# Optimization experiments

Hardware: AMD Instinct MI355X
Metric: run time of the kernel (lower is better)

The kernel has to match this reference:

```python
import jax, jax.numpy as jnp
import numpy as np

N = 10000
C = 16
AVG_DEG = 32
TAU = 1.0


def _label_propagate(adj, labels, train_mask, gumbel, iter_step, k_hop):
    # Faithful port of ContextLabel.LabelPropagate + get_label_distribution.
    m = train_mask[:, None]  # [N,1] bool
    Y = jnp.where(m, labels, jnp.zeros_like(labels))  # Y_pred init: zeros w/ train rows set
    for _ in range(iter_step):
        Y = adj @ Y                      # [N,N]@[N,C] propagation (memory-bound, C small)
        Y = jnp.where(m, labels, Y)      # masked overwrite of train rows
    if k_hop == 0:
        return Y
    # F.gumbel_softmax(Y, hard=True), tau=1: straight-through one-hot
    logits = (Y + gumbel) / TAU
    soft = jax.nn.softmax(logits, axis=-1)
    hard = jax.nn.one_hot(jnp.argmax(logits, axis=-1), C, dtype=soft.dtype)
    Y = hard + soft - jax.lax.stop_gradient(soft)
    Y = jnp.where(m, labels, Y)
    # k-hop adjacency power (loop over static k_hop-1)
    a = adj
    for _ in range(k_hop - 1):
        a = a @ adj
    # get_label_distribution: torch builds a dense [N,N,C] tensor with labels[j] at every
    # nonzero (i,j) of a, then sums over dim=1. That is exactly (a != 0).float() @ labels,
    # with no gradient through the nonzero pattern — computed without the N*N*C intermediate.
    mask = jax.lax.stop_gradient((a != 0).astype(Y.dtype))
    dist = mask @ Y  # [N,C] sum of neighbor label vectors
    dist = dist / jnp.sum(dist, axis=1, keepdims=True)
    return dist


def _make_adj(key):
    k1, k2 = jax.random.split(key)
    pattern = jax.random.uniform(k1, (N, N)) < (AVG_DEG / N)  # ~32 neighbors/row
    vals = jax.random.uniform(k2, (N, N))
    a = jnp.where(pattern, vals, 0.0).astype(jnp.float32)
    a = a.at[jnp.arange(N), jnp.arange(N)].set(1.0)  # self-loops -> no empty rows
    return a / jnp.sum(a, axis=1, keepdims=True)     # row-normalized


def setup_inputs() -> dict:
    key = jax.random.key(0)
    ka, kn, kl, km, kg1, kg2 = jax.random.split(key, 6)
    adj = _make_adj(ka)             # the (perturbed) adjacency passed to forward
    adj_norm = _make_adj(kn)        # the fixed adjacency used in __init__
    labels_int = jax.random.randint(kl, (N,), 0, C)
    labels_onehot = jax.nn.one_hot(labels_int, C, dtype=jnp.float32)
    train_mask = jax.random.uniform(km, (N,)) < 0.1
    # gumbel noise: -log(-log(U)), U clipped away from {0,1}
    def gum(k):
        u = jax.random.uniform(k, (N, C), minval=1e-6, maxval=1.0 - 1e-6)
        return -jnp.log(-jnp.log(u))
    gumbel_init = gum(kg1)
    gumbel = gum(kg2)
    # pseudo_labels = detached LabelPropagate(adj_norm, labels_onehot) from __init__
    pseudo_labels = _label_propagate(adj_norm, labels_onehot, train_mask, gumbel_init,
                                     iter_step=10, k_hop=1)
    return {"adj": adj, "labels_onehot": labels_onehot, "pseudo_labels": pseudo_labels,
            "gumbel": gumbel, "train_mask": train_mask, "iter_step": 10, "k_hop": 1}


def reference(adj, labels_onehot, pseudo_labels, gumbel, train_mask, iter_step, k_hop):
    out = _label_propagate(adj, labels_onehot, train_mask, gumbel, iter_step, k_hop)
    return jnp.mean((out - pseudo_labels) ** 2)  # F.mse_loss(..., reduction='mean')
```

## Files before the change

### kernel.cpp

```cpp
#include <hip/hip_runtime.h>

#define NN 10000
#define CC 16
#define CAP 96

__device__ __forceinline__ bool mask_at(const void* p, int i, int mode) {
    if (mode == 0) return ((const int*)p)[i] != 0;
    if (mode == 1) return ((const unsigned char*)p)[i] != 0;
    return ((const float*)p)[i] != 0.0f;
}

__global__ void detect_mask_mode(const unsigned int* __restrict__ m, int* flag) {
    __shared__ int s_int_bad, s_flt_bad;
    if (threadIdx.x == 0) { s_int_bad = 0; s_flt_bad = 0; }
    __syncthreads();
    for (int i = threadIdx.x; i < NN / 4; i += blockDim.x) {
        unsigned w = m[i];
        if (w > 1u) s_int_bad = 1;
        if (w != 0u && w != 0x3F800000u) s_flt_bad = 1;
    }
    __syncthreads();
    if (threadIdx.x == 0) {
        int mode;
        if (!s_int_bad)      mode = 0;
        else if (!s_flt_bad) mode = 2;
        else                 mode = 1;
        *flag = mode;
    }
}

__global__ __launch_bounds__(256) void build_csr(const float* __restrict__ adj,
                                                 int* __restrict__ cols,
                                                 float* __restrict__ vals,
                                                 int* __restrict__ cnt) {
    __shared__ int lcnt;
    const int row = blockIdx.x;
    if (threadIdx.x == 0) lcnt = 0;
    __syncthreads();
    const float4* rp = (const float4*)(adj + (size_t)row * NN);
    const int base = row * CAP;
    for (int i = threadIdx.x; i < NN / 4; i += 256) {
        float4 v = rp[i];
        int j = i * 4;
        if (v.x != 0.f) { int p = atomicAdd(&lcnt, 1); if (p < CAP) { cols[base+p] = j;   vals[base+p] = v.x; } }
        if (v.y != 0.f) { int p = atomicAdd(&lcnt, 1); if (p < CAP) { cols[base+p] = j+1; vals[base+p] = v.y; } }
        if (v.z != 0.f) { int p = atomicAdd(&lcnt, 1); if (p < CAP) { cols[base+p] = j+2; vals[base+p] = v.z; } }
        if (v.w != 0.f) { int p = atomicAdd(&lcnt, 1); if (p < CAP) { cols[base+p] = j+3; vals[base+p] = v.w; } }
    }
    __syncthreads();
    if (threadIdx.x == 0) cnt[row] = (lcnt < CAP) ? lcnt : CAP;
}

__global__ void init_y(const float* __restrict__ labels, const void* __restrict__ tmask,
                       const int* __restrict__ flag, float* __restrict__ Y) {
    int t = blockIdx.x * 256 + threadIdx.x;
    int row = t >> 4;
    bool m = mask_at(tmask, row, *flag);
    Y[t] = m ? labels[t] : 0.0f;
}

__global__ __launch_bounds__(256) void spmv_step(const int* __restrict__ cols,
                                                 const float* __restrict__ vals,
                                                 const int* __restrict__ cnt,
                                                 const float* __restrict__ Yin,
                                                 const float* __restrict__ labels,
                                                 const void* __restrict__ tmask,
                                                 const int* __restrict__ flag,
                                                 float* __restrict__ Yout) {
    int t = blockIdx.x * 256 + threadIdx.x;
    int row = t >> 4, c = t & 15;
    int n = cnt[row];
    const int*   cp = cols + row * CAP;
    const float* vp = vals + row * CAP;
    float acc = 0.0f;
    for (int k = 0; k < n; k++) acc = fmaf(vp[k], Yin[cp[k] * CC + c], acc);
    bool m = mask_at(tmask, row, *flag);
    Yout[t] = m ? labels[t] : acc;
}

__global__ void harden(const float* __restrict__ Yin, const float* __restrict__ gumbel,
                       const float* __restrict__ labels, const void* __restrict__ tmask,
                       const int* __restrict__ flag, float* __restrict__ Yout) {
    int row = blockIdx.x * blockDim.x + threadIdx.x;
    if (row >= NN) return;
    float l[CC];
    float mx = -1e30f;
    int am = 0;
    for (int c = 0; c < CC; c++) {
        l[c] = Yin[row * CC + c] + gumbel[row * CC + c];
        if (l[c] > mx) { mx = l[c]; am = c; }
    }
    float e[CC], s = 0.0f;
    for (int c = 0; c < CC; c++) { e[c] = expf(l[c] - mx); s += e[c]; }
    bool m = mask_at(tmask, row, *flag);
    for (int c = 0; c < CC; c++) {
        float soft = e[c] / s;
        float hard = (c == am) ? 1.0f : 0.0f;
        float y = (hard + soft) - soft;
        Yout[row * CC + c] = m ? labels[row * CC + c] : y;
    }
}

__global__ __launch_bounds__(256) void mask_spmv_loss(const int* __restrict__ cols,
                                                      const int* __restrict__ cnt,
                                                      const float* __restrict__ Y2,
                                                      const float* __restrict__ pseudo,
                                                      float* __restrict__ out) {
    int t = blockIdx.x * 256 + threadIdx.x;
    int row = t >> 4;
    int n = cnt[row];
    const int* cp = cols + row * CAP;
    float acc = 0.0f;
    for (int k = 0; k < n; k++) acc += Y2[cp[k] * CC + (t & 15)];
    float rs = acc;
    for (int off = 8; off >= 1; off >>= 1) rs += __shfl_xor(rs, off, 16);
    float v = acc / rs;
    float d = v - pseudo[t];
    float contrib = d * d * (1.0f / (NN * CC));
    for (int off = 32; off >= 1; off >>= 1) contrib += __shfl_down(contrib, off, 64);
    if ((threadIdx.x & 63) == 0) atomicAdd(out, contrib);
}

extern "C" void kernel_launch(void* const* d_in, const int* in_sizes, int n_in,
                              void* d_out, int out_size, void* d_ws, size_t ws_size,
                              hipStream_t stream) {
    const float* adj    = (const float*)d_in[0];
    const float* labels = (const float*)d_in[1];
    const float* pseudo = (const float*)d_in[2];
    const float* gumbel = (const float*)d_in[3];
    const void*  tmask  = d_in[4];

    char* ws = (char*)d_ws;
    int*   flag = (int*)(ws + 0);
    int*   cnt  = (int*)(ws + 64);
    int*   cols = (int*)(ws + 40064);
    float* vals = (float*)(ws + 3880064);
    float* Ya   = (float*)(ws + 7720064);
    float* Yb   = (float*)(ws + 8360064);

    float* outp = (float*)d_out;
    hipMemsetAsync(outp, 0, sizeof(float), stream);

    detect_mask_mode<<<1, 256, 0, stream>>>((const unsigned int*)tmask, flag);
    build_csr<<<NN, 256, 0, stream>>>(adj, cols, vals, cnt);
    init_y<<<(NN * CC) / 256, 256, 0, stream>>>(labels, tmask, flag, Ya);

    float* cur = Ya;
    float* nxt = Yb;
    for (int it = 0; it < 10; ++it) {
        spmv_step<<<(NN * CC) / 256, 256, 0, stream>>>(cols, vals, cnt, cur, labels, tmask, flag, nxt);
        float* tmp = cur; cur = nxt; nxt = tmp;
    }
    harden<<<(NN + 255) / 256, 256, 0, stream>>>(cur, gumbel, labels, tmask, flag, nxt);
    mask_spmv_loss<<<(NN * CC) / 256, 256, 0, stream>>>(cols, cnt, nxt, pseudo, outp);
}
```

Baseline: 773.1 us.

## Pack CSR entries, fuse mask detection and init, replace atomic loss reduction

Column indices and values are stored together as int2 pairs so each neighbor needs one load. Mask-mode detection moves into an extra block of build_csr, and Y initialisation is folded into a first SpMV step that reads labels directly, which removes two kernel launches and one iteration. The loss switches from a global atomicAdd plus memset to per-block partial sums and a final reduction kernel, and the inner loops get unroll pragmas. Total time is dominated by the dense 400MB adjacency scan in build_csr, which is unchanged, so these launch and gather savings are small by comparison.

```diff
diff --git a/kernel.cpp b/kernel.cpp
--- a/kernel.cpp
+++ b/kernel.cpp
@@ -3,6 +3,7 @@
 #define NN 10000
 #define CC 16
 #define CAP 96
+#define NBLK 625
 
 __device__ __forceinline__ bool mask_at(const void* p, int i, int mode) {
     if (mode == 0) return ((const int*)p)[i] != 0;
@@ -10,57 +11,71 @@
     return ((const float*)p)[i] != 0.0f;
 }
 
-__global__ void detect_mask_mode(const unsigned int* __restrict__ m, int* flag) {
-    __shared__ int s_int_bad, s_flt_bad;
-    if (threadIdx.x == 0) { s_int_bad = 0; s_flt_bad = 0; }
-    __syncthreads();
-    for (int i = threadIdx.x; i < NN / 4; i += blockDim.x) {
-        unsigned w = m[i];
-        if (w > 1u) s_int_bad = 1;
-        if (w != 0u && w != 0x3F800000u) s_flt_bad = 1;
+__global__ __launch_bounds__(256) void build_csr(const float* __restrict__ adj,
+                                                 int2* __restrict__ pack,
+                                                 int* __restrict__ cnt,
+                                                 const unsigned int* __restrict__ mask_words,
+                                                 int* __restrict__ flag) {
+    if (blockIdx.x == NN) {
+        __shared__ int s_int_bad, s_flt_bad;
+        if (threadIdx.x == 0) { s_int_bad = 0; s_flt_bad = 0; }
+        __syncthreads();
+        for (int i = threadIdx.x; i < NN / 4; i += 256) {
+            unsigned w = mask_words[i];
+            if (w > 1u) s_int_bad = 1;
+            if (w != 0u && w != 0x3F800000u) s_flt_bad = 1;
+        }
+        __syncthreads();
+        if (threadIdx.x == 0) {
+            int mode;
+            if (!s_int_bad)      mode = 0;
+            else if (!s_flt_bad) mode = 2;
+            else                 mode = 1;
+            *flag = mode;
+        }
+        return;
     }
-    __syncthreads();
-    if (threadIdx.x == 0) {
-        int mode;
-        if (!s_int_bad)      mode = 0;
-        else if (!s_flt_bad) mode = 2;
-        else                 mode = 1;
-        *flag = mode;
-    }
-}
-
-__global__ __launch_bounds__(256) void build_csr(const float* __restrict__ adj,
-                                                 int* __restrict__ cols,
-                                                 float* __restrict__ vals,
-                                                 int* __restrict__ cnt) {
     __shared__ int lcnt;
     const int row = blockIdx.x;
     if (threadIdx.x == 0) lcnt = 0;
     __syncthreads();
     const float4* rp = (const float4*)(adj + (size_t)row * NN);
-    const int base = row * CAP;
+    int2* pb = pack + row * CAP;
     for (int i = threadIdx.x; i < NN / 4; i += 256) {
         float4 v = rp[i];
         int j = i * 4;
-        if (v.x != 0.f) { int p = atomicAdd(&lcnt, 1); if (p < CAP) { cols[base+p] = j;   vals[base+p] = v.x; } }
-        if (v.y != 0.f) { int p = atomicAdd(&lcnt, 1); if (p < CAP) { cols[base+p] = j+1; vals[base+p] = v.y; } }
-        if (v.z != 0.f) { int p = atomicAdd(&lcnt, 1); if (p < CAP) { cols[base+p] = j+2; vals[base+p] = v.z; } }
-        if (v.w != 0.f) { int p = atomicAdd(&lcnt, 1); if (p < CAP) { cols[base+p] = j+3; vals[base+p] = v.w; } }
+        if (v.x != 0.f) { int p = atomicAdd(&lcnt, 1); if (p < CAP) pb[p] = make_int2(j,     __float_as_int(v.x)); }
+        if (v.y != 0.f) { int p = atomicAdd(&lcnt, 1); if (p < CAP) pb[p] = make_int2(j + 1, __float_as_int(v.y)); }
+        if (v.z != 0.f) { int p = atomicAdd(&lcnt, 1); if (p < CAP) pb[p] = make_int2(j + 2, __float_as_int(v.z)); }
+        if (v.w != 0.f) { int p = atomicAdd(&lcnt, 1); if (p < CAP) pb[p] = make_int2(j + 3, __float_as_int(v.w)); }
     }
     __syncthreads();
     if (threadIdx.x == 0) cnt[row] = (lcnt < CAP) ? lcnt : CAP;
 }
 
-__global__ void init_y(const float* __restrict__ labels, const void* __restrict__ tmask,
-                       const int* __restrict__ flag, float* __restrict__ Y) {
+__global__ __launch_bounds__(256) void spmv_first(const int2* __restrict__ pack,
+                                                  const int* __restrict__ cnt,
+                                                  const float* __restrict__ labels,
+                                                  const void* __restrict__ tmask,
+                                                  const int* __restrict__ flag,
+                                                  float* __restrict__ Yout) {
     int t = blockIdx.x * 256 + threadIdx.x;
-    int row = t >> 4;
-    bool m = mask_at(tmask, row, *flag);
-    Y[t] = m ? labels[t] : 0.0f;
+    int row = t >> 4, c = t & 15;
+    int n = cnt[row];
+    int mode = *flag;
+    const int2* pp = pack + row * CAP;
+    float acc = 0.0f;
+    #pragma unroll 4
+    for (int k = 0; k < n; k++) {
+        int2 e = pp[k];
+        float yv = mask_at(tmask, e.x, mode) ? labels[e.x * CC + c] : 0.0f;
+        acc = fmaf(__int_as_float(e.y), yv, acc);
+    }
+    bool m = mask_at(tmask, row, mode);
+    Yout[t] = m ? labels[t] : acc;
 }
 
-__global__ __launch_bounds__(256) void spmv_step(const int* __restrict__ cols,
-                                                 const float* __restrict__ vals,
+__global__ __launch_bounds__(256) void spmv_step(const int2* __restrict__ pack,
                                                  const int* __restrict__ cnt,
                                                  const float* __restrict__ Yin,
                                                  const float* __restrict__ labels,
@@ -70,10 +85,13 @@
     int t = blockIdx.x * 256 + threadIdx.x;
     int row = t >> 4, c = t & 15;
     int n = cnt[row];
-    const int*   cp = cols + row * CAP;
-    const float* vp = vals + row * CAP;
+    const int2* pp = pack + row * CAP;
     float acc = 0.0f;
-    for (int k = 0; k < n; k++) acc = fmaf(vp[k], Yin[cp[k] * CC + c], acc);
+    #pragma unroll 4
+    for (int k = 0; k < n; k++) {
+        int2 e = pp[k];
+        acc = fmaf(__int_as_float(e.y), Yin[e.x * CC + c], acc);
+    }
     bool m = mask_at(tmask, row, *flag);
     Yout[t] = m ? labels[t] : acc;
 }
@@ -101,24 +119,37 @@
     }
 }
 
-__global__ __launch_bounds__(256) void mask_spmv_loss(const int* __restrict__ cols,
+__global__ __launch_bounds__(256) void mask_spmv_loss(const int2* __restrict__ pack,
                                                       const int* __restrict__ cnt,
                                                       const float* __restrict__ Y2,
                                                       const float* __restrict__ pseudo,
-                                                      float* __restrict__ out) {
+                                                      float* __restrict__ partial) {
     int t = blockIdx.x * 256 + threadIdx.x;
-    int row = t >> 4;
+    int row = t >> 4, c = t & 15;
     int n = cnt[row];
-    const int* cp = cols + row * CAP;
+    const int2* pp = pack + row * CAP;
     float acc = 0.0f;
-    for (int k = 0; k < n; k++) acc += Y2[cp[k] * CC + (t & 15)];
+    #pragma unroll 4
+    for (int k = 0; k < n; k++) acc += Y2[pp[k].x * CC + c];
     float rs = acc;
     for (int off = 8; off >= 1; off >>= 1) rs += __shfl_xor(rs, off, 16);
-    float v = acc / rs;
-    float d = v - pseudo[t];
+    float d = acc / rs - pseudo[t];
     float contrib = d * d * (1.0f / (NN * CC));
     for (int off = 32; off >= 1; off >>= 1) contrib += __shfl_down(contrib, off, 64);
-    if ((threadIdx.x & 63) == 0) atomicAdd(out, contrib);
+    __shared__ float sw[4];
+    if ((threadIdx.x & 63) == 0) sw[threadIdx.x >> 6] = contrib;
+    __syncthreads();
+    if (threadIdx.x == 0) partial[blockIdx.x] = sw[0] + sw[1] + sw[2] + sw[3];
+}
+
+__global__ void final_reduce(const float* __restrict__ partial, float* __restrict__ out) {
+    float s = 0.0f;
+    for (int i = threadIdx.x; i < NBLK; i += 256) s += partial[i];
+    for (int off = 32; off >= 1; off >>= 1) s += __shfl_down(s, off, 64);
+    __shared__ float sw[4];
+    if ((threadIdx.x & 63) == 0) sw[threadIdx.x >> 6] = s;
+    __syncthreads();
+    if (threadIdx.x == 0) out[0] = sw[0] + sw[1] + sw[2] + sw[3];
 }
 
 extern "C" void kernel_launch(void* const* d_in, const int* in_sizes, int n_in,
@@ -131,26 +162,25 @@
     const void*  tmask  = d_in[4];
 
     char* ws = (char*)d_ws;
-    int*   flag = (int*)(ws + 0);
-    int*   cnt  = (int*)(ws + 64);
-    int*   cols = (int*)(ws + 40064);
-    float* vals = (float*)(ws + 3880064);
-    float* Ya   = (float*)(ws + 7720064);
-    float* Yb   = (float*)(ws + 8360064);
+    int*   flag    = (int*)(ws + 0);
+    int*   cnt     = (int*)(ws + 64);
+    int2*  pack    = (int2*)(ws + 40064);
+    float* Ya      = (float*)(ws + 7720064);
+    float* Yb      = (float*)(ws + 8360064);
+    float* partial = (float*)(ws + 9000064);
 
     float* outp = (float*)d_out;
-    hipMemsetAsync(outp, 0, sizeof(float), stream);
 
-    detect_mask_mode<<<1, 256, 0, stream>>>((const unsigned int*)tmask, flag);
-    build_csr<<<NN, 256, 0, stream>>>(adj, cols, vals, cnt);
-    init_y<<<(NN * CC) / 256, 256, 0, stream>>>(labels, tmask, flag, Ya);
+    build_csr<<<NN + 1, 256, 0, stream>>>(adj, pack, cnt, (const unsigned int*)tmask, flag);
 
+    spmv_first<<<NBLK, 256, 0, stream>>>(pack, cnt, labels, tmask, flag, Ya);
     float* cur = Ya;
     float* nxt = Yb;
-    for (int it = 0; it < 10; ++it) {
-        spmv_step<<<(NN * CC) / 256, 256, 0, stream>>>(cols, vals, cnt, cur, labels, tmask, flag, nxt);
+    for (int it = 0; it < 9; ++it) {
+        spmv_step<<<NBLK, 256, 0, stream>>>(pack, cnt, cur, labels, tmask, flag, nxt);
         float* tmp = cur; cur = nxt; nxt = tmp;
     }
     harden<<<(NN + 255) / 256, 256, 0, stream>>>(cur, gumbel, labels, tmask, flag, nxt);
-    mask_spmv_loss<<<(NN * CC) / 256, 256, 0, stream>>>(cols, cnt, nxt, pseudo, outp);
+    mask_spmv_loss<<<NBLK, 256, 0, stream>>>(pack, cnt, nxt, pseudo, partial);
+    final_reduce<<<1, 256, 0, stream>>>(partial, outp);
 }
```

Result: faster. 636.9 us (-17.6%).
